# Performance work log

Hardware: AMD Instinct MI355X
Metric: run time of the kernel (lower is better)

The kernel has to match this reference:

```python
import jax, jax.numpy as jnp
import numpy as np
import math

D_MODEL = 1024
NUM_HEADS = 16
D_K = D_MODEL // NUM_HEADS
SEQ = 2048
BATCH = 2


def setup_inputs() -> dict:
    key = jax.random.key(0)
    ks = jax.random.split(key, 11)
    s = 1.0 / math.sqrt(D_MODEL)
    return {
        "query": jax.random.normal(ks[0], (SEQ, BATCH, D_MODEL), jnp.float32),
        "key": jax.random.normal(ks[1], (SEQ, BATCH, D_MODEL), jnp.float32),
        "value": jax.random.normal(ks[2], (SEQ, BATCH, D_MODEL), jnp.float32),
        "Wq": jax.random.normal(ks[3], (D_MODEL, D_MODEL), jnp.float32) * s,
        "bq": jnp.zeros((D_MODEL,), jnp.float32),
        "Wk": jax.random.normal(ks[4], (D_MODEL, D_MODEL), jnp.float32) * s,
        "bk": jnp.zeros((D_MODEL,), jnp.float32),
        "Wv": jax.random.normal(ks[5], (D_MODEL, D_MODEL), jnp.float32) * s,
        "bv": jnp.zeros((D_MODEL,), jnp.float32),
        "Wo": jax.random.normal(ks[6], (D_MODEL, D_MODEL), jnp.float32) * s,
        "bo": jnp.zeros((D_MODEL,), jnp.float32),
    }


def _split_heads(x):
    # [S, B, D] -> [S, B, H, d_k]
    S, B, _ = x.shape
    return x.reshape(S, B, NUM_HEADS, D_K)


def reference(query, key, value, Wq, bq, Wk, bk, Wv, bv, Wo, bo):
    # torch Linear: y = x @ W.T + b
    q = _split_heads(query @ Wq.T + bq)   # [S,B,H,dk]
    k = _split_heads(key @ Wk.T + bk)
    v = _split_heads(value @ Wv.T + bv)
    # score[q,k,b,h] = sum_d q[q,b,h,d] k[k,b,h,d]
    score = jnp.einsum('qbhd,kbhd->qkbh', q, k) / math.sqrt(D_K)
    attn = jax.nn.softmax(score, axis=1)  # Softmax(dim=1) == over key axis
    out = jnp.einsum('qkbh,kbhd->qbhd', attn, v)  # [S,B,H,dk]
    S, B = out.shape[0], out.shape[1]
    out = out.reshape(S, B, NUM_HEADS * D_K)
    return out @ Wo.T + bo
```

## Files before the change

### kernel.cpp

```cpp
#include <hip/hip_runtime.h>

typedef unsigned short u16;
typedef short s16x8 __attribute__((ext_vector_type(8)));
typedef short s16x4 __attribute__((ext_vector_type(4)));
typedef float f32x4 __attribute__((ext_vector_type(4)));

#define MFMA_BF16(A,B,C) __builtin_amdgcn_mfma_f32_16x16x32_bf16(A,B,C,0,0,0)

#if defined(__has_builtin)
#if __has_builtin(__builtin_amdgcn_mfma_f32_16x16x16bf16_1k)
#define HAVE_MFMA16 1
#define MFMA16(A,B,C) __builtin_amdgcn_mfma_f32_16x16x16bf16_1k(A,B,C,0,0,0)
#endif
#endif

static constexpr int DMODEL = 1024;
static constexpr int SEQn   = 2048;
static constexpr int BATCH  = 2;
static constexpr int NH     = 16;
static constexpr int DKn    = 64;
static constexpr int ROWST  = BATCH*DMODEL;
static constexpr float QSCALE = 0.18033688011112042f;

__device__ __forceinline__ u16 f2bf(float f) {
    unsigned u = __builtin_bit_cast(unsigned, f);
    u += 0x7FFFu + ((u >> 16) & 1u);
    return (u16)(u >> 16);
}

#if defined(__has_builtin)
#if __has_builtin(__builtin_amdgcn_cvt_pk_bf16_f32)
#define HAVE_PKBF16 1
#endif
#endif
#ifdef HAVE_PKBF16
typedef __bf16 bf16x2 __attribute__((ext_vector_type(2)));
__device__ __forceinline__ unsigned pk2bf(float a, float b) {
    bf16x2 t = __builtin_amdgcn_cvt_pk_bf16_f32(a, b);
    return __builtin_bit_cast(unsigned, t);
}
#else
__device__ __forceinline__ unsigned pk2bf(float a, float b) {
    return (unsigned)f2bf(a) | ((unsigned)f2bf(b) << 16);
}
#endif

__device__ __forceinline__ void gld_lds16(const u16* g, u16* l) {
    __builtin_amdgcn_global_load_lds(
        (const __attribute__((address_space(1))) void*)g,
        (__attribute__((address_space(3))) void*)l,
        16, 0, 0);
}

__global__ void cvt_bf16(const float* __restrict__ q, const float* __restrict__ k,
                         const float* __restrict__ v, const float* __restrict__ wq,
                         const float* __restrict__ wk, const float* __restrict__ wv,
                         const float* __restrict__ wo,
                         u16* __restrict__ qb, u16* __restrict__ kb, u16* __restrict__ vb,
                         u16* __restrict__ wqb, u16* __restrict__ wkb, u16* __restrict__ wvb,
                         u16* __restrict__ wob)
{
    const int z = blockIdx.z;
    const float* S; u16* D; size_t n;
    switch (z) {
        case 0: S = q;  D = qb;  n = 4194304; break;
        case 1: S = k;  D = kb;  n = 4194304; break;
        case 2: S = v;  D = vb;  n = 4194304; break;
        case 3: S = wq; D = wqb; n = 1048576; break;
        case 4: S = wk; D = wkb; n = 1048576; break;
        case 5: S = wv; D = wvb; n = 1048576; break;
        default: S = wo; D = wob; n = 1048576; break;
    }
    const size_t i = ((size_t)blockIdx.x * 256 + threadIdx.x) * 8;
    if (i >= n) return;
    float4 a = *(const float4*)(S + i);
    float4 b = *(const float4*)(S + i + 4);
    uint4 pk;
    pk.x = pk2bf(a.x, a.y); pk.y = pk2bf(a.z, a.w);
    pk.z = pk2bf(b.x, b.y); pk.w = pk2bf(b.z, b.w);
    *(uint4*)(D + i) = pk;
}

template<bool FINAL>
__global__ __launch_bounds__(256, 3)
void gemm_p(const u16* __restrict__ A0, const u16* __restrict__ A1, const u16* __restrict__ A2,
            const u16* __restrict__ W0, const u16* __restrict__ W1, const u16* __restrict__ W2,
            const float* __restrict__ B0, const float* __restrict__ B1, const float* __restrict__ B2,
            void* __restrict__ O0, void* __restrict__ O1, void* __restrict__ O2)
{
    const u16* A; const u16* W; const float* bias; void* Outv;
    const int z = blockIdx.z;
    if (z == 0)      { A = A0; W = W0; bias = B0; Outv = O0; }
    else if (z == 1) { A = A1; W = W1; bias = B1; Outv = O1; }
    else             { A = A2; W = W2; bias = B2; Outv = O2; }

    __shared__ alignas(16) u16 SH[24576];

    const int tid  = threadIdx.x;
    const int wave = tid >> 6, lane = tid & 63;
    const int quad = lane >> 4, col = lane & 15;
    const int wm = wave & 1, wn = wave >> 1;
    const int m0 = blockIdx.y * 128, n0 = blockIdx.x * 128;

    f32x4 acc[4][4];
#pragma unroll
    for (int i = 0; i < 4; ++i)
#pragma unroll
        for (int j = 0; j < 4; ++j) acc[i][j] = f32x4{0.f,0.f,0.f,0.f};

    auto stageT = [&](int t) {
        const int slot = t % 3;
        const int k0 = t * 32;
        u16* Ad = SH + slot*4096;
        u16* Bd = SH + 12288 + slot*4096;
#pragma unroll
        for (int i = 0; i < 2; ++i) {
            const int idx = i*256 + wave*64 + lane;
            const int row = idx >> 2;
            const int g = (idx & 3) ^ ((row >> 1) & 3);
            gld_lds16(A + (size_t)(m0 + row)*DMODEL + k0 + g*8, Ad + (i*256 + wave*64)*8);
            gld_lds16(W + (size_t)(n0 + row)*DMODEL + k0 + g*8, Bd + (i*256 + wave*64)*8);
        }
    };

    auto compute = [&](int slot) {
        const u16* As_ = SH + slot*4096;
        const u16* Bs_ = SH + 12288 + slot*4096;
        s16x8 af[4], bfr[4];
#pragma unroll
        for (int t4 = 0; t4 < 4; ++t4) {
            const int ra = wm*64 + t4*16 + col;
            af[t4]  = *(const s16x8*)&As_[ra*32 + ((quad ^ ((ra >> 1) & 3))*8)];
            const int rb = wn*64 + t4*16 + col;
            bfr[t4] = *(const s16x8*)&Bs_[rb*32 + ((quad ^ ((rb >> 1) & 3))*8)];
        }
        __builtin_amdgcn_s_setprio(1);
#pragma unroll
        for (int i = 0; i < 4; ++i)
#pragma unroll
            for (int j = 0; j < 4; ++j)
                acc[i][j] = MFMA_BF16(af[i], bfr[j], acc[i][j]);
        __builtin_amdgcn_s_setprio(0);
    };

    stageT(0); stageT(1);

    for (int t = 0; t < 31; ++t) {
        asm volatile("s_waitcnt vmcnt(4)" ::: "memory");
        __builtin_amdgcn_s_barrier();
        asm volatile("" ::: "memory");
        if (t < 30) stageT(t + 2);
        compute(t % 3);
    }
    asm volatile("s_waitcnt vmcnt(0)" ::: "memory");
    __builtin_amdgcn_s_barrier();
    asm volatile("" ::: "memory");
    compute(31 % 3);

    float bv[4];
#pragma unroll
    for (int j = 0; j < 4; ++j) bv[j] = bias[n0 + wn*64 + j*16 + col];

    if (FINAL) {
#pragma unroll
        for (int i = 0; i < 4; ++i)
#pragma unroll
            for (int j = 0; j < 4; ++j) {
                const int n = n0 + wn*64 + j*16 + col;
#pragma unroll
                for (int r = 0; r < 4; ++r) {
                    const int m = m0 + wm*64 + i*16 + quad*4 + r;
                    ((float*)Outv)[(size_t)m*DMODEL + n] = acc[i][j][r] + bv[j];
                }
            }
    } else {
        const float osc = (z == 0) ? QSCALE : 1.f;
        const int SST = (z == 2) ? 129 : 128;
        __syncthreads();
#pragma unroll
        for (int i = 0; i < 4; ++i)
#pragma unroll
            for (int j = 0; j < 4; ++j) {
                const int nl = wn*64 + j*16 + col;
#pragma unroll
                for (int r = 0; r < 4; ++r) {
                    const int ml = wm*64 + i*16 + quad*4 + r;
                    SH[ml*SST + nl] = f2bf((acc[i][j][r] + bv[j])*osc);
                }
            }
        __syncthreads();
        u16* Out = (u16*)Outv;
        if (z < 2) {
#pragma unroll
            for (int t = 0; t < 8; ++t) {
                const int c = t*256 + tid;
                const int ml = c >> 4, n8 = (c & 15)*8;
                uint4 x = *(const uint4*)&SH[ml*128 + n8];
                *(uint4*)(Out + (size_t)(m0 + ml)*DMODEL + n0 + n8) = x;
            }
        } else {
            const int s0 = m0 >> 1;
#pragma unroll
            for (int t = 0; t < 8; ++t) {
                const int c = t*256 + tid;
                const int sc = c & 7;
                const int nl = (c >> 3) & 127;
                const int bb = c >> 10;
                u16 e[8];
#pragma unroll
                for (int j = 0; j < 8; ++j)
                    e[j] = SH[((sc*8 + j)*2 + bb)*129 + nl];
                uint4 x; __builtin_memcpy(&x, e, 16);
                const int ng = n0 + nl, hh = ng >> 6, dd = ng & 63;
                *(uint4*)(Out + (((size_t)bb*NH + hh)*DKn + dd)*SEQn + s0 + sc*8) = x;
            }
        }
    }
}

__global__ __launch_bounds__(256, 4)
void attn_fwd(const u16* __restrict__ Q, const u16* __restrict__ K,
              const u16* __restrict__ Vt, u16* __restrict__ O)
{
    __shared__ alignas(16) u16 Ks[128*64];
    __shared__ alignas(16) u16 Vs[64*128];

    const int qt = blockIdx.x, bh = blockIdx.y;
    const int b = bh >> 4, h = bh & 15;
    const int tid = threadIdx.x;
    const int wave = tid >> 6, lane = tid & 63;
    const int quad = lane >> 4, col = lane & 15;

    const u16* Qh = Q + b*DMODEL + h*DKn;
    const u16* Kh = K + b*DMODEL + h*DKn;
    const u16* Vh = Vt + (size_t)bh*DKn*SEQn;

    const int q0 = qt*64 + wave*16;
    s16x8 qf[2];
#pragma unroll
    for (int ks = 0; ks < 2; ++ks)
        qf[ks] = *(const s16x8*)(Qh + (size_t)(q0 + col)*ROWST + ks*32 + quad*8);

    const short ONEBF = (short)0x3F80;
    const s16x4 ones = {ONEBF, ONEBF, ONEBF, ONEBF};

    f32x4 o[4];
    f32x4 lacc = f32x4{0.f,0.f,0.f,0.f};
#pragma unroll
    for (int dt = 0; dt < 4; ++dt) o[dt] = f32x4{0.f,0.f,0.f,0.f};

    for (int kt = 0; kt < SEQn/128; ++kt) {
        __syncthreads();
#pragma unroll
        for (int i = 0; i < 4; ++i) {
            {
                const int chunk = (i*4 + wave)*64 + lane;
                const int row = chunk >> 3;
                const int kk = ((chunk & 7) ^ (row & 7))*8;
                gld_lds16(Kh + (size_t)(kt*128 + row)*ROWST + kk, &Ks[(i*4 + wave)*512]);
            }
            {
                const int chunk = (i*4 + wave)*64 + lane;
                const int d = chunk >> 4;
                const int kk = ((chunk & 15) ^ (d & 15))*8;
                gld_lds16(Vh + (size_t)d*SEQn + kt*128 + kk, &Vs[(i*4 + wave)*512]);
            }
        }
        __syncthreads();

        f32x4 sfr[8];
#pragma unroll
        for (int nt = 0; nt < 8; ++nt) sfr[nt] = f32x4{0.f,0.f,0.f,0.f};
#pragma unroll
        for (int ks = 0; ks < 2; ++ks) {
            s16x8 kf[8];
#pragma unroll
            for (int nt = 0; nt < 8; ++nt) {
                const int key = nt*16 + col;
                kf[nt] = *(const s16x8*)&Ks[key*64 + (((ks*4 + quad) ^ (key & 7))*8)];
            }
#pragma unroll
            for (int nt = 0; nt < 8; ++nt)
                sfr[nt] = MFMA_BF16(kf[nt], qf[ks], sfr[nt]);
        }

        s16x4 pk[8];
#pragma unroll
        for (int nt = 0; nt < 8; ++nt) {
            float p0 = __builtin_amdgcn_exp2f(sfr[nt][0]);
            float p1 = __builtin_amdgcn_exp2f(sfr[nt][1]);
            float p2 = __builtin_amdgcn_exp2f(sfr[nt][2]);
            float p3 = __builtin_amdgcn_exp2f(sfr[nt][3]);
            unsigned w[2] = { pk2bf(p0, p1), pk2bf(p2, p3) };
            __builtin_memcpy(&pk[nt], w, 8);
        }

#ifdef HAVE_MFMA16
#pragma unroll
        for (int c = 0; c < 8; ++c) {
            lacc = MFMA16(ones, pk[c], lacc);
#pragma unroll
            for (int dt = 0; dt < 4; ++dt) {
                const int d = dt*16 + col;
                const s16x4 vfr = *(const s16x4*)&Vs[d*128 + (((c*2 + (quad>>1)) ^ (d & 15))*8) + (quad & 1)*4];
                o[dt] = MFMA16(vfr, pk[c], o[dt]);
            }
        }
#else
        const int a0 = (32*(quad & 1) + col)*4;
        const s16x8 ones8 = {ONEBF,ONEBF,ONEBF,ONEBF,ONEBF,ONEBF,ONEBF,ONEBF};
#pragma unroll
        for (int ksp = 0; ksp < 4; ++ksp) {
            int pA[2], pB[2];
            __builtin_memcpy(pA, &pk[ksp*2], 8);
            __builtin_memcpy(pB, &pk[ksp*2 + 1], 8);
            int w[4];
#pragma unroll
            for (int hh = 0; hh < 2; ++hh) {
                const int ad = a0 + hh*64;
                const int xA0 = __builtin_amdgcn_ds_bpermute(ad, pA[0]);
                const int xA1 = __builtin_amdgcn_ds_bpermute(ad, pA[1]);
                const int xB0 = __builtin_amdgcn_ds_bpermute(ad, pB[0]);
                const int xB1 = __builtin_amdgcn_ds_bpermute(ad, pB[1]);
                w[hh*2]     = (quad >= 2) ? xB0 : xA0;
                w[hh*2 + 1] = (quad >= 2) ? xB1 : xA1;
            }
            s16x8 pfr; __builtin_memcpy(&pfr, w, 16);
            lacc = MFMA_BF16(ones8, pfr, lacc);
#pragma unroll
            for (int dt = 0; dt < 4; ++dt) {
                const int d = dt*16 + col;
                const s16x8 vfr = *(const s16x8*)&Vs[d*128 + (((ksp*4 + quad) ^ (d & 15))*8)];
                o[dt] = MFMA_BF16(vfr, pfr, o[dt]);
            }
        }
#endif
    }

    const float inv = 1.f / lacc[0];
    const int srow = q0 + col;
#pragma unroll
    for (int dt = 0; dt < 4; ++dt) {
        uint2 pko;
        pko.x = pk2bf(o[dt][0]*inv, o[dt][1]*inv);
        pko.y = pk2bf(o[dt][2]*inv, o[dt][3]*inv);
        *(uint2*)(O + ((size_t)srow*BATCH + b)*DMODEL + h*DKn + dt*16 + quad*4) = pko;
    }
}

extern "C" void kernel_launch(void* const* d_in, const int* in_sizes, int n_in,
                              void* d_out, int out_size, void* d_ws, size_t ws_size,
                              hipStream_t stream)
{
    const float* q  = (const float*)d_in[0];
    const float* k  = (const float*)d_in[1];
    const float* v  = (const float*)d_in[2];
    const float* Wq = (const float*)d_in[3];
    const float* bq = (const float*)d_in[4];
    const float* Wk = (const float*)d_in[5];
    const float* bk = (const float*)d_in[6];
    const float* Wv = (const float*)d_in[7];
    const float* bv = (const float*)d_in[8];
    const float* Wo = (const float*)d_in[9];
    const float* bo = (const float*)d_in[10];
    float* out = (float*)d_out;

    const size_t N = (size_t)SEQn * BATCH * DMODEL;
    const size_t NW = (size_t)DMODEL * DMODEL;
    u16* qb  = (u16*)d_ws;
    u16* kb  = qb + N;
    u16* vb  = kb + N;
    u16* wqb = vb + N;
    u16* wkb = wqb + NW;
    u16* wvb = wkb + NW;
    u16* wob = wvb + NW;
    u16* Qw  = wob + NW;
    u16* Kw  = Qw + N;
    u16* Vtw = Kw + N;
    u16* AO  = qb;

    cvt_bf16<<<dim3(2048, 1, 7), 256, 0, stream>>>(q, k, v, Wq, Wk, Wv, Wo,
                                                   qb, kb, vb, wqb, wkb, wvb, wob);
    gemm_p<false><<<dim3(8, 32, 3), 256, 0, stream>>>(qb, kb, vb, wqb, wkb, wvb,
                                                      bq, bk, bv, Qw, Kw, Vtw);
    attn_fwd<<<dim3(32, 32), 256, 0, stream>>>(Qw, Kw, Vtw, AO);
    gemm_p<true><<<dim3(8, 32, 1), 256, 0, stream>>>(AO, AO, AO, wob, wob, wob,
                                                     bo, bo, bo, out, out, out);
}
```

Before: 224.2 us.

## Fuse fp32-to-bf16 activation conversion into QKV projection GEMM loads

Result: slower. 239.3 us (+6.7%).

```diff
diff --git a/kernel.cpp b/kernel.cpp
--- a/kernel.cpp
+++ b/kernel.cpp
@@ -52,27 +52,15 @@
         16, 0, 0);
 }
 
-__global__ void cvt_bf16(const float* __restrict__ q, const float* __restrict__ k,
-                         const float* __restrict__ v, const float* __restrict__ wq,
-                         const float* __restrict__ wk, const float* __restrict__ wv,
-                         const float* __restrict__ wo,
-                         u16* __restrict__ qb, u16* __restrict__ kb, u16* __restrict__ vb,
-                         u16* __restrict__ wqb, u16* __restrict__ wkb, u16* __restrict__ wvb,
-                         u16* __restrict__ wob)
+__global__ void cvt_w(const float* __restrict__ w0, const float* __restrict__ w1,
+                      const float* __restrict__ w2, const float* __restrict__ w3,
+                      u16* __restrict__ o0, u16* __restrict__ o1,
+                      u16* __restrict__ o2, u16* __restrict__ o3)
 {
     const int z = blockIdx.z;
-    const float* S; u16* D; size_t n;
-    switch (z) {
-        case 0: S = q;  D = qb;  n = 4194304; break;
-        case 1: S = k;  D = kb;  n = 4194304; break;
-        case 2: S = v;  D = vb;  n = 4194304; break;
-        case 3: S = wq; D = wqb; n = 1048576; break;
-        case 4: S = wk; D = wkb; n = 1048576; break;
-        case 5: S = wv; D = wvb; n = 1048576; break;
-        default: S = wo; D = wob; n = 1048576; break;
-    }
+    const float* S = (z == 0) ? w0 : (z == 1) ? w1 : (z == 2) ? w2 : w3;
+    u16* D        = (z == 0) ? o0 : (z == 1) ? o1 : (z == 2) ? o2 : o3;
     const size_t i = ((size_t)blockIdx.x * 256 + threadIdx.x) * 8;
-    if (i >= n) return;
     float4 a = *(const float4*)(S + i);
     float4 b = *(const float4*)(S + i + 4);
     uint4 pk;
@@ -81,19 +69,165 @@
     *(uint4*)(D + i) = pk;
 }
 
-template<bool FINAL>
 __global__ __launch_bounds__(256, 3)
-void gemm_p(const u16* __restrict__ A0, const u16* __restrict__ A1, const u16* __restrict__ A2,
-            const u16* __restrict__ W0, const u16* __restrict__ W1, const u16* __restrict__ W2,
-            const float* __restrict__ B0, const float* __restrict__ B1, const float* __restrict__ B2,
-            void* __restrict__ O0, void* __restrict__ O1, void* __restrict__ O2)
+void gemm_qkv(const float* __restrict__ A0f, const float* __restrict__ A1f,
+              const float* __restrict__ A2f,
+              const u16* __restrict__ W0, const u16* __restrict__ W1, const u16* __restrict__ W2,
+              const float* __restrict__ B0, const float* __restrict__ B1, const float* __restrict__ B2,
+              u16* __restrict__ O0, u16* __restrict__ O1, u16* __restrict__ O2)
 {
-    const u16* A; const u16* W; const float* bias; void* Outv;
+    const float* Af; const u16* W; const float* bias; u16* Out;
     const int z = blockIdx.z;
-    if (z == 0)      { A = A0; W = W0; bias = B0; Outv = O0; }
-    else if (z == 1) { A = A1; W = W1; bias = B1; Outv = O1; }
-    else             { A = A2; W = W2; bias = B2; Outv = O2; }
-
+    if (z == 0)      { Af = A0f; W = W0; bias = B0; Out = O0; }
+    else if (z == 1) { Af = A1f; W = W1; bias = B1; Out = O1; }
+    else             { Af = A2f; W = W2; bias = B2; Out = O2; }
+
+    __shared__ alignas(16) u16 SH[24576];
+
+    const int tid  = threadIdx.x;
+    const int wave = tid >> 6, lane = tid & 63;
+    const int quad = lane >> 4, col = lane & 15;
+    const int wm = wave & 1, wn = wave >> 1;
+    const int m0 = blockIdx.y * 128, n0 = blockIdx.x * 128;
+
+    f32x4 acc[4][4];
+#pragma unroll
+    for (int i = 0; i < 4; ++i)
+#pragma unroll
+        for (int j = 0; j < 4; ++j) acc[i][j] = f32x4{0.f,0.f,0.f,0.f};
+
+    auto stageW = [&](int t) {
+        const int slot = t % 3;
+        const int k0 = t * 32;
+        u16* Bd = SH + 12288 + slot*4096;
+#pragma unroll
+        for (int i = 0; i < 2; ++i) {
+            const int idx = i*256 + wave*64 + lane;
+            const int row = idx >> 2;
+            const int g = (idx & 3) ^ ((row >> 1) & 3);
+            gld_lds16(W + (size_t)(n0 + row)*DMODEL + k0 + g*8, Bd + (i*256 + wave*64)*8);
+        }
+    };
+    auto issueA = [&](int t, float4* r) {
+        const int k0 = t * 32;
+#pragma unroll
+        for (int i = 0; i < 2; ++i) {
+            const int idx = i*256 + wave*64 + lane;
+            const int row = idx >> 2;
+            const int g = (idx & 3) ^ ((row >> 1) & 3);
+            const float* src = Af + (size_t)(m0 + row)*DMODEL + k0 + g*8;
+            r[i*2]     = *(const float4*)(src);
+            r[i*2 + 1] = *(const float4*)(src + 4);
+        }
+    };
+    auto writeA = [&](int t, const float4* r) {
+        const int slot = t % 3;
+        u16* Ad = SH + slot*4096;
+#pragma unroll
+        for (int i = 0; i < 2; ++i) {
+            uint4 pk;
+            pk.x = pk2bf(r[i*2].x, r[i*2].y);
+            pk.y = pk2bf(r[i*2].z, r[i*2].w);
+            pk.z = pk2bf(r[i*2 + 1].x, r[i*2 + 1].y);
+            pk.w = pk2bf(r[i*2 + 1].z, r[i*2 + 1].w);
+            *(uint4*)(Ad + (i*256 + wave*64 + lane)*8) = pk;
+        }
+    };
+    auto compute = [&](int slot) {
+        const u16* As_ = SH + slot*4096;
+        const u16* Bs_ = SH + 12288 + slot*4096;
+        s16x8 af[4], bfr[4];
+#pragma unroll
+        for (int t4 = 0; t4 < 4; ++t4) {
+            const int ra = wm*64 + t4*16 + col;
+            af[t4]  = *(const s16x8*)&As_[ra*32 + ((quad ^ ((ra >> 1) & 3))*8)];
+            const int rb = wn*64 + t4*16 + col;
+            bfr[t4] = *(const s16x8*)&Bs_[rb*32 + ((quad ^ ((rb >> 1) & 3))*8)];
+        }
+        __builtin_amdgcn_s_setprio(1);
+#pragma unroll
+        for (int i = 0; i < 4; ++i)
+#pragma unroll
+            for (int j = 0; j < 4; ++j)
+                acc[i][j] = MFMA_BF16(af[i], bfr[j], acc[i][j]);
+        __builtin_amdgcn_s_setprio(0);
+    };
+
+    float4 ra[4], rb[4];
+    issueA(0, ra); stageW(0);
+    issueA(1, rb); stageW(1);
+    writeA(0, ra);
+    asm volatile("s_waitcnt vmcnt(6) lgkmcnt(0)" ::: "memory");
+    __builtin_amdgcn_s_barrier();
+
+    for (int t = 0; t < 30; t += 2) {
+        issueA(t + 2, ra); stageW(t + 2);
+        writeA(t + 1, rb);
+        compute(t % 3);
+        asm volatile("s_waitcnt vmcnt(6) lgkmcnt(0)" ::: "memory");
+        __builtin_amdgcn_s_barrier();
+        issueA(t + 3, rb); stageW(t + 3);
+        writeA(t + 2, ra);
+        compute((t + 1) % 3);
+        asm volatile("s_waitcnt vmcnt(6) lgkmcnt(0)" ::: "memory");
+        __builtin_amdgcn_s_barrier();
+    }
+    writeA(31, rb);
+    compute(30 % 3);
+    asm volatile("s_waitcnt vmcnt(0) lgkmcnt(0)" ::: "memory");
+    __builtin_amdgcn_s_barrier();
+    compute(31 % 3);
+
+    float bv[4];
+#pragma unroll
+    for (int j = 0; j < 4; ++j) bv[j] = bias[n0 + wn*64 + j*16 + col];
+
+    const float osc = (z == 0) ? QSCALE : 1.f;
+    const int SST = (z == 2) ? 129 : 128;
+    __syncthreads();
+#pragma unroll
+    for (int i = 0; i < 4; ++i)
+#pragma unroll
+        for (int j = 0; j < 4; ++j) {
+            const int nl = wn*64 + j*16 + col;
+#pragma unroll
+            for (int r = 0; r < 4; ++r) {
+                const int ml = wm*64 + i*16 + quad*4 + r;
+                SH[ml*SST + nl] = f2bf((acc[i][j][r] + bv[j])*osc);
+            }
+        }
+    __syncthreads();
+    if (z < 2) {
+#pragma unroll
+        for (int t = 0; t < 8; ++t) {
+            const int c = t*256 + tid;
+            const int ml = c >> 4, n8 = (c & 15)*8;
+            uint4 x = *(const uint4*)&SH[ml*128 + n8];
+            *(uint4*)(Out + (size_t)(m0 + ml)*DMODEL + n0 + n8) = x;
+        }
+    } else {
+        const int s0 = m0 >> 1;
+#pragma unroll
+        for (int t = 0; t < 8; ++t) {
+            const int c = t*256 + tid;
+            const int sc = c & 7;
+            const int nl = (c >> 3) & 127;
+            const int bb = c >> 10;
+            u16 e[8];
+#pragma unroll
+            for (int j = 0; j < 8; ++j)
+                e[j] = SH[((sc*8 + j)*2 + bb)*129 + nl];
+            uint4 x; __builtin_memcpy(&x, e, 16);
+            const int ng = n0 + nl, hh = ng >> 6, dd = ng & 63;
+            *(uint4*)(Out + (((size_t)bb*NH + hh)*DKn + dd)*SEQn + s0 + sc*8) = x;
+        }
+    }
+}
+
+__global__ __launch_bounds__(256, 3)
+void gemm_fin(const u16* __restrict__ A, const u16* __restrict__ W,
+              const float* __restrict__ bias, float* __restrict__ Outv)
+{
     __shared__ alignas(16) u16 SH[24576];
 
     const int tid  = threadIdx.x;
@@ -122,7 +256,6 @@
             gld_lds16(W + (size_t)(n0 + row)*DMODEL + k0 + g*8, Bd + (i*256 + wave*64)*8);
         }
     };
-
     auto compute = [&](int slot) {
         const u16* As_ = SH + slot*4096;
         const u16* Bs_ = SH + 12288 + slot*4096;
@@ -144,7 +277,6 @@
     };
 
     stageT(0); stageT(1);
-
     for (int t = 0; t < 31; ++t) {
         asm volatile("s_waitcnt vmcnt(4)" ::: "memory");
         __builtin_amdgcn_s_barrier();
@@ -160,62 +292,17 @@
     float bv[4];
 #pragma unroll
     for (int j = 0; j < 4; ++j) bv[j] = bias[n0 + wn*64 + j*16 + col];
-
-    if (FINAL) {
-#pragma unroll
-        for (int i = 0; i < 4; ++i)
-#pragma unroll
-            for (int j = 0; j < 4; ++j) {
-                const int n = n0 + wn*64 + j*16 + col;
-#pragma unroll
-                for (int r = 0; r < 4; ++r) {
-                    const int m = m0 + wm*64 + i*16 + quad*4 + r;
-                    ((float*)Outv)[(size_t)m*DMODEL + n] = acc[i][j][r] + bv[j];
-                }
-            }
-    } else {
-        const float osc = (z == 0) ? QSCALE : 1.f;
-        const int SST = (z == 2) ? 129 : 128;
-        __syncthreads();
-#pragma unroll
-        for (int i = 0; i < 4; ++i)
-#pragma unroll
-            for (int j = 0; j < 4; ++j) {
-                const int nl = wn*64 + j*16 + col;
-#pragma unroll
-                for (int r = 0; r < 4; ++r) {
-                    const int ml = wm*64 + i*16 + quad*4 + r;
-                    SH[ml*SST + nl] = f2bf((acc[i][j][r] + bv[j])*osc);
-                }
-            }
-        __syncthreads();
-        u16* Out = (u16*)Outv;
-        if (z < 2) {
-#pragma unroll
-            for (int t = 0; t < 8; ++t) {
-                const int c = t*256 + tid;
-                const int ml = c >> 4, n8 = (c & 15)*8;
-                uint4 x = *(const uint4*)&SH[ml*128 + n8];
-                *(uint4*)(Out + (size_t)(m0 + ml)*DMODEL + n0 + n8) = x;
-            }
-        } else {
-            const int s0 = m0 >> 1;
-#pragma unroll
-            for (int t = 0; t < 8; ++t) {
-                const int c = t*256 + tid;
-                const int sc = c & 7;
-                const int nl = (c >> 3) & 127;
-                const int bb = c >> 10;
-                u16 e[8];
-#pragma unroll
-                for (int j = 0; j < 8; ++j)
-                    e[j] = SH[((sc*8 + j)*2 + bb)*129 + nl];
-                uint4 x; __builtin_memcpy(&x, e, 16);
-                const int ng = n0 + nl, hh = ng >> 6, dd = ng & 63;
-                *(uint4*)(Out + (((size_t)bb*NH + hh)*DKn + dd)*SEQn + s0 + sc*8) = x;
-            }
-        }
-    }
+#pragma unroll
+    for (int i = 0; i < 4; ++i)
+#pragma unroll
+        for (int j = 0; j < 4; ++j) {
+            const int n = n0 + wn*64 + j*16 + col;
+#pragma unroll
+            for (int r = 0; r < 4; ++r) {
+                const int m = m0 + wm*64 + i*16 + quad*4 + r;
+                Outv[(size_t)m*DMODEL + n] = acc[i][j][r] + bv[j];
+            }
+        }
 }
 
 __global__ __launch_bounds__(256, 4)
@@ -367,23 +454,18 @@
 
     const size_t N = (size_t)SEQn * BATCH * DMODEL;
     const size_t NW = (size_t)DMODEL * DMODEL;
-    u16* qb  = (u16*)d_ws;
-    u16* kb  = qb + N;
-    u16* vb  = kb + N;
-    u16* wqb = vb + N;
+    u16* wqb = (u16*)d_ws;
     u16* wkb = wqb + NW;
     u16* wvb = wkb + NW;
     u16* wob = wvb + NW;
     u16* Qw  = wob + NW;
     u16* Kw  = Qw + N;
     u16* Vtw = Kw + N;
-    u16* AO  = qb;
-
-    cvt_bf16<<<dim3(2048, 1, 7), 256, 0, stream>>>(q, k, v, Wq, Wk, Wv, Wo,
-                                                   qb, kb, vb, wqb, wkb, wvb, wob);
-    gemm_p<false><<<dim3(8, 32, 3), 256, 0, stream>>>(qb, kb, vb, wqb, wkb, wvb,
-                                                      bq, bk, bv, Qw, Kw, Vtw);
+    u16* AO  = Vtw + N;
+
+    cvt_w<<<dim3(512, 1, 4), 256, 0, stream>>>(Wq, Wk, Wv, Wo, wqb, wkb, wvb, wob);
+    gemm_qkv<<<dim3(8, 32, 3), 256, 0, stream>>>(q, k, v, wqb, wkb, wvb,
+                                                 bq, bk, bv, Qw, Kw, Vtw);
     attn_fwd<<<dim3(32, 32), 256, 0, stream>>>(Qw, Kw, Vtw, AO);
-    gemm_p<true><<<dim3(8, 32, 1), 256, 0, stream>>>(AO, AO, AO, wob, wob, wob,
-                                                     bo, bo, bo, out, out, out);
-}
+    gemm_fin<<<dim3(8, 32, 1), 256, 0, stream>>>(AO, wob, bo, out);
+}
```
